# Kernel optimization log

Measured on AMD Instinct MI355X. Metric: run time of the kernel, lower is better.

The kernel has to match this reference:

```python
import jax, jax.numpy as jnp
import numpy as np

EPS = 1e-5

def _add_self_loops(edge_index, n):
    loop = jnp.arange(n, dtype=edge_index.dtype)
    return jnp.concatenate([edge_index, jnp.stack([loop, loop])], axis=1)

def _gcn_norm(row, col, n, dtype):
    # degree of target nodes (with self loops, unit edge weights)
    deg = jax.ops.segment_sum(jnp.ones(row.shape[0], dtype=dtype), col, num_segments=n)
    dinv = jnp.where(deg > 0, deg ** -0.5, 0.0).astype(dtype)
    return dinv[row] * dinv[col]  # [E]

def _propagate(xw, row, col, ew, n):
    # gather -> scale -> scatter-add
    msgs = ew[:, None] * xw[row]          # [E, C]
    return jax.ops.segment_sum(msgs, col, num_segments=n)  # [N, C]

def _batchnorm(x, gamma, beta):
    mu = jnp.mean(x, axis=0)
    var = jnp.var(x, axis=0)
    return (x - mu) * jax.lax.rsqrt(var + EPS) * gamma + beta

def setup_inputs() -> dict:
    key = jax.random.key(0)
    ks = jax.random.split(key, 10)
    N, C_in, C_h, C_out, E = 50000, 128, 128, 1, 600000
    x = jax.random.normal(ks[0], (N, C_in), dtype=jnp.float32)
    edge_index = jax.random.randint(ks[1], (2, E), 0, N, dtype=jnp.int64)
    s = 1.0 / np.sqrt(C_in)
    return {
        "x": x,
        "edge_index": edge_index,
        "gcn_w": jax.random.uniform(ks[2], (C_in, C_h), jnp.float32, -s, s),
        "gcn_b": jnp.zeros((C_h,), jnp.float32),
        "bn1_g": jnp.ones((C_h,), jnp.float32),
        "bn1_b": jnp.zeros((C_h,), jnp.float32),
        "dcn_w": jax.random.uniform(ks[3], (C_h, C_h), jnp.float32, -s, s),
        "dcn_b": jnp.zeros((C_h,), jnp.float32),
        "bn3_g": jnp.ones((C_h,), jnp.float32),
        "bn3_b": jnp.zeros((C_h,), jnp.float32),
        "out_w": jax.random.uniform(ks[4], (2 * C_h, C_out), jnp.float32, -s, s),
        "out_b": jnp.zeros((C_out,), jnp.float32),
    }

def reference(x, edge_index, gcn_w, gcn_b, bn1_g, bn1_b, dcn_w, dcn_b, bn3_g, bn3_b, out_w, out_b):
    n = x.shape[0]
    ei = _add_self_loops(edge_index, n)
    row, col = ei[0], ei[1]
    ew = _gcn_norm(row, col, n, x.dtype)

    # GCNConv: lin -> normalized aggregate -> bias
    h = _propagate(x @ gcn_w, row, col, ew, n) + gcn_b
    h = _batchnorm(h, bn1_g, bn1_b)

    # DegGNNConv: lin -> normalized aggregate -> elementwise gate with input -> bias
    out = _propagate(h @ dcn_w, row, col, ew, n)
    out = out * h + dcn_b
    out = _batchnorm(out, bn3_g, bn3_b)
    # dropout is identity in eval mode

    xc = jnp.concatenate([h, out], axis=-1)  # [N, 2*C_h]
    return xc @ out_w + out_b
```

## Files before the change

kernel.cpp:

```cpp
#include <hip/hip_runtime.h>
#include <hip/hip_bf16.h>
#include <cstdint>


typedef __attribute__((ext_vector_type(8))) short bf16x8;
typedef __attribute__((ext_vector_type(4))) float f32x4;

__device__ __forceinline__ ushort f2bf(float f) {
    union { float f; unsigned u; } c; c.f = f;
    unsigned u = c.u;
    return (ushort)((u + 0x7fffu + ((u >> 16) & 1u)) >> 16);
}
__device__ __forceinline__ unsigned pack2bf(float a, float b) {
    return (unsigned)f2bf(a) | ((unsigned)f2bf(b) << 16);
}
__device__ __forceinline__ float bflo(unsigned u) {
    union { unsigned i; float f; } c; c.i = u << 16; return c.f;
}
__device__ __forceinline__ float bfhi(unsigned u) {
    union { unsigned i; float f; } c; c.i = u & 0xffff0000u; return c.f;
}

__global__ void zero_kernel(uint4* __restrict__ p, int nwords) {
    int i = blockIdx.x * blockDim.x + threadIdx.x;
    if (i < nwords) p[i] = (uint4){0u, 0u, 0u, 0u};
}

__global__ void convert_kernel(const void* __restrict__ ei, int E,
                               int* __restrict__ count) {
    const int* e32 = (const int*)ei;
    bool is64 = ((e32[1] | e32[3] | e32[5] | e32[7]) == 0);
    int stride = gridDim.x * blockDim.x;
    for (int e = blockIdx.x * blockDim.x + threadIdx.x; e < E; e += stride) {
        int c = is64 ? (int)((const long long*)ei)[E + e] : e32[E + e];
        atomicAdd(&count[c], 1);
    }
}

__global__ __launch_bounds__(256) void bsum_kernel(const int* __restrict__ count,
                                                   int* __restrict__ bsum, int n) {
    int t = threadIdx.x;
    int i0 = blockIdx.x * 1024 + t * 4;
    int s = 0;
    if (i0 + 4 <= n) {
        int4 v = *(const int4*)&count[i0];
        s = v.x + v.y + v.z + v.w;
    } else {
        for (int i = i0; i < n; i++) s += count[i];
    }
    __shared__ int ls[256];
    ls[t] = s;
    __syncthreads();
    for (int off = 128; off > 0; off >>= 1) {
        if (t < off) ls[t] += ls[t + off];
        __syncthreads();
    }
    if (t == 0) bsum[blockIdx.x] = ls[0];
}

__global__ void scanb_kernel(int* __restrict__ bsum, int nb) {
    __shared__ int sm[1024];
    int t = threadIdx.x;
    int v = (t < nb) ? bsum[t] : 0;
    sm[t] = v;
    __syncthreads();
    for (int off = 1; off < 1024; off <<= 1) {
        int a = (t >= off) ? sm[t - off] : 0;
        __syncthreads();
        sm[t] += a;
        __syncthreads();
    }
    if (t < nb) bsum[t] = sm[t] - v;
}

__global__ __launch_bounds__(256) void emit_kernel(const int* __restrict__ count,
                                                   const int* __restrict__ bbase,
                                                   int* __restrict__ base, int n) {
    int t = threadIdx.x;
    int i0 = blockIdx.x * 1024 + t * 4;
    int v[4];
    int s = 0;
    if (i0 + 4 <= n) {
        int4 q = *(const int4*)&count[i0];
        v[0] = q.x; v[1] = q.y; v[2] = q.z; v[3] = q.w;
        s = v[0] + v[1] + v[2] + v[3];
    } else {
        #pragma unroll
        for (int k = 0; k < 4; k++) {
            int i = i0 + k;
            v[k] = (i < n) ? count[i] : 0;
            s += v[k];
        }
    }
    __shared__ int sm[256];
    sm[t] = s;
    __syncthreads();
    for (int off = 1; off < 256; off <<= 1) {
        int a = (t >= off) ? sm[t - off] : 0;
        __syncthreads();
        sm[t] += a;
        __syncthreads();
    }
    int run = bbase[blockIdx.x] + sm[t] - s;
    #pragma unroll
    for (int k = 0; k < 4; k++) {
        int i = i0 + k;
        if (i < n) {
            base[i] = run;
            run += v[k];
        }
    }
}

__global__ void scatter_kernel(const void* __restrict__ ei, int E,
                               const int* __restrict__ base, int* __restrict__ cursor,
                               const int* __restrict__ count,
                               unsigned* __restrict__ esrc) {
    const int* e32 = (const int*)ei;
    bool is64 = ((e32[1] | e32[3] | e32[5] | e32[7]) == 0);
    int stride = gridDim.x * blockDim.x;
    for (int e = blockIdx.x * blockDim.x + threadIdx.x; e < E; e += stride) {
        int r, c;
        if (is64) {
            r = (int)((const long long*)ei)[e];
            c = (int)((const long long*)ei)[E + e];
        } else {
            r = e32[e];
            c = e32[E + e];
        }
        int pos = base[c] + atomicAdd(&cursor[c], 1);
        unsigned deg = (unsigned)count[r];
        esrc[pos] = (deg << 24) | ((unsigned)r << 6);
    }
}

__global__ void wtrans_kernel(const float* __restrict__ W1, ushort* __restrict__ WT1,
                              const float* __restrict__ W2, ushort* __restrict__ WT2) {
    int b = blockIdx.x;
    const float* W = (b < 64) ? W1 : W2;
    ushort* WT = (b < 64) ? WT1 : WT2;
    int t = (b & 63) * 256 + threadIdx.x;
    int c = t >> 7, k = t & 127;
    WT[t] = f2bf(W[k * 128 + c]);
}

__global__ __launch_bounds__(256) void gemm_mfma_kernel(const float* __restrict__ Xf,
                                                        const ushort* __restrict__ Xb,
                                                        const ushort* __restrict__ WT,
                                                        const float* __restrict__ ab,
                                                        ushort* __restrict__ Ybf, int n) {
    __shared__ ushort Wl[128 * 136];
    int t = threadIdx.x;
    for (int idx = t * 8; idx < 128 * 128; idx += 256 * 8) {
        int c = idx >> 7;
        int k = idx & 127;
        *(uint4*)&Wl[c * 136 + k] = *(const uint4*)&WT[idx];
    }
    __syncthreads();

    int wid = t >> 6;
    int lane = t & 63;
    int m0 = blockIdx.x * 64 + wid * 16;
    if (m0 >= n) return;
    int row = m0 + (lane & 15);
    int rc = row < n ? row : n - 1;
    int kg = (lane >> 4) * 8;

    f32x4 acc[8];
    #pragma unroll
    for (int i = 0; i < 8; i++) acc[i] = (f32x4){0.f, 0.f, 0.f, 0.f};

    #pragma unroll
    for (int ks = 0; ks < 4; ks++) {
        int k0 = ks * 32 + kg;
        bf16x8 a;
        if (Xb) {
            uint4 q = *(const uint4*)&Xb[(size_t)rc * 128 + k0];
            float f0 = bflo(q.x), f1 = bfhi(q.x), f2 = bflo(q.y), f3 = bfhi(q.y);
            float f4 = bflo(q.z), f5 = bfhi(q.z), f6 = bflo(q.w), f7 = bfhi(q.w);
            float4 alo = *(const float4*)&ab[k0];
            float4 ahi = *(const float4*)&ab[k0 + 4];
            float4 blo = *(const float4*)&ab[128 + k0];
            float4 bhi = *(const float4*)&ab[128 + k0 + 4];
            a[0] = (short)f2bf(alo.x * f0 + blo.x);
            a[1] = (short)f2bf(alo.y * f1 + blo.y);
            a[2] = (short)f2bf(alo.z * f2 + blo.z);
            a[3] = (short)f2bf(alo.w * f3 + blo.w);
            a[4] = (short)f2bf(ahi.x * f4 + bhi.x);
            a[5] = (short)f2bf(ahi.y * f5 + bhi.y);
            a[6] = (short)f2bf(ahi.z * f6 + bhi.z);
            a[7] = (short)f2bf(ahi.w * f7 + bhi.w);
        } else {
            const float* xr = &Xf[(size_t)rc * 128];
            float4 lo = *(const float4*)&xr[k0];
            float4 hi = *(const float4*)&xr[k0 + 4];
            a[0] = (short)f2bf(lo.x); a[1] = (short)f2bf(lo.y);
            a[2] = (short)f2bf(lo.z); a[3] = (short)f2bf(lo.w);
            a[4] = (short)f2bf(hi.x); a[5] = (short)f2bf(hi.y);
            a[6] = (short)f2bf(hi.z); a[7] = (short)f2bf(hi.w);
        }
        #pragma unroll
        for (int nt = 0; nt < 8; nt++) {
            int c = nt * 16 + (lane & 15);
            bf16x8 b = *(bf16x8*)&Wl[c * 136 + k0];
            acc[nt] = __builtin_amdgcn_mfma_f32_16x16x32_bf16(a, b, acc[nt], 0, 0, 0);
        }
    }

    int ro = m0 + (lane >> 4) * 4;
    int co = lane & 15;
    #pragma unroll
    for (int nt = 0; nt < 8; nt++) {
        #pragma unroll
        for (int i = 0; i < 4; i++) {
            int r = ro + i;
            if (r < n) Ybf[(size_t)r * 128 + nt * 16 + co] = f2bf(acc[nt][i]);
        }
    }
}

__global__ __launch_bounds__(256) void prop_kernel(const uint4* __restrict__ XW4,
                            const int* __restrict__ base,
                            const int* __restrict__ count, const unsigned* __restrict__ esrc,
                            const uint4* __restrict__ B1q, const float* __restrict__ ab1,
                            uint4* __restrict__ outq,
                            float* __restrict__ psum, float* __restrict__ psq,
                            int n, int gate) {
    int wave4 = (int)((blockIdx.x * blockDim.x + threadIdx.x) >> 6);
    int lane = threadIdx.x & 63;
    int wid = threadIdx.x >> 6;
    int g = lane >> 4;
    int p = lane & 15;
    int node = wave4 * 4 + g;
    bool valid = node < n;
    int nc = valid ? node : n - 1;
    int b = 0, cnt = 0;
    if (valid) { b = base[node]; cnt = count[node]; }
    float din = rsqrtf((float)(cnt + 1));

    uint4 vs = XW4[(size_t)nc * 16 + p];

    float ax[8];
    #pragma unroll
    for (int k = 0; k < 8; k++) ax[k] = 0.f;

    for (int i = 0; i < cnt; i += 4) {
        unsigned pj[4];
        uint4 vj[4];
        #pragma unroll
        for (int j = 0; j < 4; j++) {
            int e = i + j;
            pj[j] = esrc[b + (e < cnt ? e : cnt - 1)];
        }
        #pragma unroll
        for (int j = 0; j < 4; j++)
            vj[j] = XW4[((pj[j] & 0xFFFFFFu) >> 2) + p];
        #pragma unroll
        for (int j = 0; j < 4; j++) {
            float w = (i + j < cnt) ? rsqrtf((float)((pj[j] >> 24) + 1)) : 0.f;
            ax[0] += w * bflo(vj[j].x); ax[1] += w * bfhi(vj[j].x);
            ax[2] += w * bflo(vj[j].y); ax[3] += w * bfhi(vj[j].y);
            ax[4] += w * bflo(vj[j].z); ax[5] += w * bfhi(vj[j].z);
            ax[6] += w * bflo(vj[j].w); ax[7] += w * bfhi(vj[j].w);
        }
    }

    float sv[8];
    sv[0] = bflo(vs.x); sv[1] = bfhi(vs.x); sv[2] = bflo(vs.y); sv[3] = bfhi(vs.y);
    sv[4] = bflo(vs.z); sv[5] = bfhi(vs.z); sv[6] = bflo(vs.w); sv[7] = bfhi(vs.w);
    #pragma unroll
    for (int k = 0; k < 8; k++) ax[k] = din * (ax[k] + din * sv[k]);

    float vv[8];
    if (gate) {
        uint4 b1 = B1q[(size_t)nc * 16 + p];
        float bv[8];
        bv[0] = bflo(b1.x); bv[1] = bfhi(b1.x); bv[2] = bflo(b1.y); bv[3] = bfhi(b1.y);
        bv[4] = bflo(b1.z); bv[5] = bfhi(b1.z); bv[6] = bflo(b1.w); bv[7] = bfhi(b1.w);
        int c0 = p * 8;
        #pragma unroll
        for (int k = 0; k < 8; k++) {
            float h = ab1[c0 + k] * bv[k] + ab1[128 + c0 + k];
            vv[k] = ax[k] * h;
        }
    } else {
        #pragma unroll
        for (int k = 0; k < 8; k++) vv[k] = ax[k];
    }

    if (valid) {
        uint4 o;
        o.x = pack2bf(vv[0], vv[1]);
        o.y = pack2bf(vv[2], vv[3]);
        o.z = pack2bf(vv[4], vv[5]);
        o.w = pack2bf(vv[6], vv[7]);
        outq[(size_t)node * 16 + p] = o;
    } else {
        #pragma unroll
        for (int k = 0; k < 8; k++) vv[k] = 0.f;
    }

    float ss[8], qq[8];
    #pragma unroll
    for (int k = 0; k < 8; k++) { ss[k] = vv[k]; qq[k] = vv[k] * vv[k]; }
    #pragma unroll
    for (int k = 0; k < 8; k++) {
        ss[k] += __shfl_xor(ss[k], 16); qq[k] += __shfl_xor(qq[k], 16);
        ss[k] += __shfl_xor(ss[k], 32); qq[k] += __shfl_xor(qq[k], 32);
    }
    __shared__ float sm_s[4][128], sm_q[4][128];
    if (g == 0) {
        int c0 = p * 8;
        #pragma unroll
        for (int k = 0; k < 8; k++) {
            sm_s[wid][c0 + k] = ss[k];
            sm_q[wid][c0 + k] = qq[k];
        }
    }
    __syncthreads();
    if (threadIdx.x < 128) {
        int c = threadIdx.x;
        float s = sm_s[0][c] + sm_s[1][c] + sm_s[2][c] + sm_s[3][c];
        float q2 = sm_q[0][c] + sm_q[1][c] + sm_q[2][c] + sm_q[3][c];
        int slot = (blockIdx.x & 63) * 128;
        atomicAdd(&psum[slot + c], s);
        atomicAdd(&psq[slot + c], q2);
    }
}

__global__ void reduce_ab_kernel(const float* __restrict__ psum, const float* __restrict__ psq,
                                 const float* __restrict__ g, const float* __restrict__ beta,
                                 float* __restrict__ ab, int n) {
    int c = threadIdx.x;
    float s = 0.f, s2 = 0.f;
    for (int r = 0; r < 64; r++) {
        s += psum[r * 128 + c];
        s2 += psq[r * 128 + c];
    }
    float invn = 1.f / (float)n;
    float mu = s * invn;
    float var = s2 * invn - mu * mu;
    float a = g[c] * rsqrtf(var + 1e-5f);
    ab[c] = a;
    ab[128 + c] = beta[c] - mu * a;
}

__global__ void final_kernel(const unsigned* __restrict__ B1bf, const unsigned* __restrict__ B2bf,
                             const float* __restrict__ ab1, const float* __restrict__ ab3,
                             const float* __restrict__ ow, const float* __restrict__ ob,
                             float* __restrict__ out, int n) {
    int wave = (int)((blockIdx.x * blockDim.x + threadIdx.x) >> 6);
    int lane = threadIdx.x & 63;
    if (wave >= n) return;
    int c0 = 2 * lane, c1 = c0 + 1;
    unsigned b1 = B1bf[(size_t)wave * 64 + lane];
    unsigned b2 = B2bf[(size_t)wave * 64 + lane];
    float h0 = ab1[c0] * bflo(b1) + ab1[128 + c0];
    float h1 = ab1[c1] * bfhi(b1) + ab1[128 + c1];
    float o0 = ab3[c0] * bflo(b2) + ab3[128 + c0];
    float o1 = ab3[c1] * bfhi(b2) + ab3[128 + c1];
    float partial = h0 * ow[c0] + h1 * ow[c1] + o0 * ow[128 + c0] + o1 * ow[128 + c1];
    #pragma unroll
    for (int off = 32; off > 0; off >>= 1) partial += __shfl_down(partial, off);
    if (lane == 0) out[wave] = partial + ob[0];
}

extern "C" void kernel_launch(void* const* d_in, const int* in_sizes, int n_in,
                              void* d_out, int out_size, void* d_ws, size_t ws_size,
                              hipStream_t stream) {
    const float* x     = (const float*)d_in[0];
    const void*  ei    = d_in[1];
    const float* gcn_w = (const float*)d_in[2];
    const float* bn1_g = (const float*)d_in[4];
    const float* bn1_b = (const float*)d_in[5];
    const float* dcn_w = (const float*)d_in[6];
    const float* bn3_g = (const float*)d_in[8];
    const float* bn3_b = (const float*)d_in[9];
    const float* out_w = (const float*)d_in[10];
    const float* out_b = (const float*)d_in[11];
    float* out = (float*)d_out;

    int N = in_sizes[0] / 128;
    int E = in_sizes[1] / 2;
    size_t N128 = (size_t)N * 128;

    ushort* Abf   = (ushort*)d_ws;
    ushort* B1bf  = Abf + N128;
    ushort* B2bf  = B1bf + N128;
    unsigned* esrc = (unsigned*)(B2bf + N128);
    int*   base  = (int*)(esrc + E);
    int*   bsum  = base + N;
    ushort* WT1  = (ushort*)(bsum + 1024);
    ushort* WT2  = WT1 + 16384;
    float* ab1   = (float*)(WT2 + 16384);
    float* ab3   = ab1 + 256;
    int*   count  = (int*)(ab3 + 256);
    int*   cursor = count + N;
    float* psum1  = (float*)(cursor + N);
    float* psq1   = psum1 + 8192;
    float* psum3  = psq1 + 8192;
    float* psq3   = psum3 + 8192;

    size_t zero_bytes = (size_t)((char*)(psq3 + 8192) - (char*)count);
    int zwords = (int)(zero_bytes / 16);
    zero_kernel<<<(zwords + 255) / 256, 256, 0, stream>>>((uint4*)count, zwords);

    int egrid = (E + 255) / 256;
    if (egrid > 2048) egrid = 2048;
    int nb = (N + 1023) / 1024;
    int ggrid = (N + 63) / 64;
    int pgrid = (N + 15) / 16;
    int fgrid = (N + 3) / 4;

    convert_kernel<<<egrid, 256, 0, stream>>>(ei, E, count);
    bsum_kernel<<<nb, 256, 0, stream>>>(count, bsum, N);
    scanb_kernel<<<1, 1024, 0, stream>>>(bsum, nb);
    emit_kernel<<<nb, 256, 0, stream>>>(count, bsum, base, N);
    scatter_kernel<<<egrid, 256, 0, stream>>>(ei, E, base, cursor, count, esrc);
    wtrans_kernel<<<128, 256, 0, stream>>>(gcn_w, WT1, dcn_w, WT2);

    gemm_mfma_kernel<<<ggrid, 256, 0, stream>>>(x, nullptr, WT1, nullptr, Abf, N);
    prop_kernel<<<pgrid, 256, 0, stream>>>((const uint4*)Abf, base, count, esrc,
                                           nullptr, nullptr, (uint4*)B1bf,
                                           psum1, psq1, N, 0);
    reduce_ab_kernel<<<1, 128, 0, stream>>>(psum1, psq1, bn1_g, bn1_b, ab1, N);

    gemm_mfma_kernel<<<ggrid, 256, 0, stream>>>(nullptr, B1bf, WT2, ab1, Abf, N);
    prop_kernel<<<pgrid, 256, 0, stream>>>((const uint4*)Abf, base, count, esrc,
                                           (const uint4*)B1bf, ab1, (uint4*)B2bf,
                                           psum3, psq3, N, 1);
    reduce_ab_kernel<<<1, 128, 0, stream>>>(psum3, psq3, bn3_g, bn3_b, ab3, N);

    final_kernel<<<fgrid, 256, 0, stream>>>((const unsigned*)B1bf, (const unsigned*)B2bf,
                                            ab1, ab3, out_w, out_b, out, N);
}
```

Measured before the change: 172.2 us.

## Merge independent setup kernels into heterogeneous launches and drop cursor array

The weight transpose now runs as extra blocks inside the degree-count kernel. The edge scatter and the first GEMM share one launch, with block index choosing the role. The separate cursor array is gone: scatter atomically bumps base[c] directly, and prop recovers the start offset as base minus count. This cuts launches and serialization gaps and lets the GEMM overlap the atomic-bound scatter. In exchange, the fused kernel carries GEMM shared-memory usage into the scatter blocks, which may reduce their occupancy.

```diff
diff --git a/kernel.cpp b/kernel.cpp
--- a/kernel.cpp
+++ b/kernel.cpp
@@ -26,12 +26,23 @@
     if (i < nwords) p[i] = (uint4){0u, 0u, 0u, 0u};
 }
 
-__global__ void convert_kernel(const void* __restrict__ ei, int E,
-                               int* __restrict__ count) {
+__global__ void fuse1_kernel(const void* __restrict__ ei, int E,
+                             int* __restrict__ count, int cgrid,
+                             const float* __restrict__ W1, ushort* __restrict__ WT1,
+                             const float* __restrict__ W2, ushort* __restrict__ WT2) {
+    if (blockIdx.x >= cgrid) {
+        int b = blockIdx.x - cgrid;
+        const float* W = (b < 64) ? W1 : W2;
+        ushort* WT = (b < 64) ? WT1 : WT2;
+        int t = (b & 63) * 256 + threadIdx.x;
+        int c = t >> 7, k = t & 127;
+        WT[t] = f2bf(W[k * 128 + c]);
+        return;
+    }
     const int* e32 = (const int*)ei;
     bool is64 = ((e32[1] | e32[3] | e32[5] | e32[7]) == 0);
-    int stride = gridDim.x * blockDim.x;
-    for (int e = blockIdx.x * blockDim.x + threadIdx.x; e < E; e += stride) {
+    int stride = cgrid * 256;
+    for (int e = blockIdx.x * 256 + threadIdx.x; e < E; e += stride) {
         int c = is64 ? (int)((const long long*)ei)[E + e] : e32[E + e];
         atomicAdd(&count[c], 1);
     }
@@ -112,40 +123,84 @@
     }
 }
 
-__global__ void scatter_kernel(const void* __restrict__ ei, int E,
-                               const int* __restrict__ base, int* __restrict__ cursor,
-                               const int* __restrict__ count,
-                               unsigned* __restrict__ esrc) {
-    const int* e32 = (const int*)ei;
-    bool is64 = ((e32[1] | e32[3] | e32[5] | e32[7]) == 0);
-    int stride = gridDim.x * blockDim.x;
-    for (int e = blockIdx.x * blockDim.x + threadIdx.x; e < E; e += stride) {
-        int r, c;
-        if (is64) {
-            r = (int)((const long long*)ei)[e];
-            c = (int)((const long long*)ei)[E + e];
-        } else {
-            r = e32[e];
-            c = e32[E + e];
-        }
-        int pos = base[c] + atomicAdd(&cursor[c], 1);
-        unsigned deg = (unsigned)count[r];
-        esrc[pos] = (deg << 24) | ((unsigned)r << 6);
-    }
-}
-
-__global__ void wtrans_kernel(const float* __restrict__ W1, ushort* __restrict__ WT1,
-                              const float* __restrict__ W2, ushort* __restrict__ WT2) {
-    int b = blockIdx.x;
-    const float* W = (b < 64) ? W1 : W2;
-    ushort* WT = (b < 64) ? WT1 : WT2;
-    int t = (b & 63) * 256 + threadIdx.x;
-    int c = t >> 7, k = t & 127;
-    WT[t] = f2bf(W[k * 128 + c]);
-}
-
-__global__ __launch_bounds__(256) void gemm_mfma_kernel(const float* __restrict__ Xf,
-                                                        const ushort* __restrict__ Xb,
+__global__ __launch_bounds__(256) void fuse2_kernel(const void* __restrict__ ei, int E,
+                             int* __restrict__ base, const int* __restrict__ count,
+                             unsigned* __restrict__ esrc, int sgrid,
+                             const float* __restrict__ Xf, const ushort* __restrict__ WT,
+                             ushort* __restrict__ Ybf, int n) {
+    __shared__ ushort Wl[128 * 136];
+    if (blockIdx.x < sgrid) {
+        const int* e32 = (const int*)ei;
+        bool is64 = ((e32[1] | e32[3] | e32[5] | e32[7]) == 0);
+        int stride = sgrid * 256;
+        for (int e = blockIdx.x * 256 + threadIdx.x; e < E; e += stride) {
+            int r, c;
+            if (is64) {
+                r = (int)((const long long*)ei)[e];
+                c = (int)((const long long*)ei)[E + e];
+            } else {
+                r = e32[e];
+                c = e32[E + e];
+            }
+            int pos = atomicAdd(&base[c], 1);
+            unsigned deg = (unsigned)count[r];
+            esrc[pos] = (deg << 24) | ((unsigned)r << 6);
+        }
+        return;
+    }
+    int gb = blockIdx.x - sgrid;
+    int t = threadIdx.x;
+    for (int idx = t * 8; idx < 128 * 128; idx += 256 * 8) {
+        int c = idx >> 7;
+        int k = idx & 127;
+        *(uint4*)&Wl[c * 136 + k] = *(const uint4*)&WT[idx];
+    }
+    __syncthreads();
+
+    int wid = t >> 6;
+    int lane = t & 63;
+    int m0 = gb * 64 + wid * 16;
+    if (m0 >= n) return;
+    int row = m0 + (lane & 15);
+    int rc = row < n ? row : n - 1;
+    int kg = (lane >> 4) * 8;
+
+    f32x4 acc[8];
+    #pragma unroll
+    for (int i = 0; i < 8; i++) acc[i] = (f32x4){0.f, 0.f, 0.f, 0.f};
+
+    #pragma unroll
+    for (int ks = 0; ks < 4; ks++) {
+        int k0 = ks * 32 + kg;
+        const float* xr = &Xf[(size_t)rc * 128];
+        float4 lo = *(const float4*)&xr[k0];
+        float4 hi = *(const float4*)&xr[k0 + 4];
+        bf16x8 a;
+        a[0] = (short)f2bf(lo.x); a[1] = (short)f2bf(lo.y);
+        a[2] = (short)f2bf(lo.z); a[3] = (short)f2bf(lo.w);
+        a[4] = (short)f2bf(hi.x); a[5] = (short)f2bf(hi.y);
+        a[6] = (short)f2bf(hi.z); a[7] = (short)f2bf(hi.w);
+        #pragma unroll
+        for (int nt = 0; nt < 8; nt++) {
+            int c = nt * 16 + (lane & 15);
+            bf16x8 b = *(bf16x8*)&Wl[c * 136 + k0];
+            acc[nt] = __builtin_amdgcn_mfma_f32_16x16x32_bf16(a, b, acc[nt], 0, 0, 0);
+        }
+    }
+
+    int ro = m0 + (lane >> 4) * 4;
+    int co = lane & 15;
+    #pragma unroll
+    for (int nt = 0; nt < 8; nt++) {
+        #pragma unroll
+        for (int i = 0; i < 4; i++) {
+            int r = ro + i;
+            if (r < n) Ybf[(size_t)r * 128 + nt * 16 + co] = f2bf(acc[nt][i]);
+        }
+    }
+}
+
+__global__ __launch_bounds__(256) void gemm_mfma_kernel(const ushort* __restrict__ Xb,
                                                         const ushort* __restrict__ WT,
                                                         const float* __restrict__ ab,
                                                         ushort* __restrict__ Ybf, int n) {
@@ -173,32 +228,22 @@
     #pragma unroll
     for (int ks = 0; ks < 4; ks++) {
         int k0 = ks * 32 + kg;
+        uint4 q = *(const uint4*)&Xb[(size_t)rc * 128 + k0];
+        float f0 = bflo(q.x), f1 = bfhi(q.x), f2 = bflo(q.y), f3 = bfhi(q.y);
+        float f4 = bflo(q.z), f5 = bfhi(q.z), f6 = bflo(q.w), f7 = bfhi(q.w);
+        float4 alo = *(const float4*)&ab[k0];
+        float4 ahi = *(const float4*)&ab[k0 + 4];
+        float4 blo = *(const float4*)&ab[128 + k0];
+        float4 bhi = *(const float4*)&ab[128 + k0 + 4];
         bf16x8 a;
-        if (Xb) {
-            uint4 q = *(const uint4*)&Xb[(size_t)rc * 128 + k0];
-            float f0 = bflo(q.x), f1 = bfhi(q.x), f2 = bflo(q.y), f3 = bfhi(q.y);
-            float f4 = bflo(q.z), f5 = bfhi(q.z), f6 = bflo(q.w), f7 = bfhi(q.w);
-            float4 alo = *(const float4*)&ab[k0];
-            float4 ahi = *(const float4*)&ab[k0 + 4];
-            float4 blo = *(const float4*)&ab[128 + k0];
-            float4 bhi = *(const float4*)&ab[128 + k0 + 4];
-            a[0] = (short)f2bf(alo.x * f0 + blo.x);
-            a[1] = (short)f2bf(alo.y * f1 + blo.y);
-            a[2] = (short)f2bf(alo.z * f2 + blo.z);
-            a[3] = (short)f2bf(alo.w * f3 + blo.w);
-            a[4] = (short)f2bf(ahi.x * f4 + bhi.x);
-            a[5] = (short)f2bf(ahi.y * f5 + bhi.y);
-            a[6] = (short)f2bf(ahi.z * f6 + bhi.z);
-            a[7] = (short)f2bf(ahi.w * f7 + bhi.w);
-        } else {
-            const float* xr = &Xf[(size_t)rc * 128];
-            float4 lo = *(const float4*)&xr[k0];
-            float4 hi = *(const float4*)&xr[k0 + 4];
-            a[0] = (short)f2bf(lo.x); a[1] = (short)f2bf(lo.y);
-            a[2] = (short)f2bf(lo.z); a[3] = (short)f2bf(lo.w);
-            a[4] = (short)f2bf(hi.x); a[5] = (short)f2bf(hi.y);
-            a[6] = (short)f2bf(hi.z); a[7] = (short)f2bf(hi.w);
-        }
+        a[0] = (short)f2bf(alo.x * f0 + blo.x);
+        a[1] = (short)f2bf(alo.y * f1 + blo.y);
+        a[2] = (short)f2bf(alo.z * f2 + blo.z);
+        a[3] = (short)f2bf(alo.w * f3 + blo.w);
+        a[4] = (short)f2bf(ahi.x * f4 + bhi.x);
+        a[5] = (short)f2bf(ahi.y * f5 + bhi.y);
+        a[6] = (short)f2bf(ahi.z * f6 + bhi.z);
+        a[7] = (short)f2bf(ahi.w * f7 + bhi.w);
         #pragma unroll
         for (int nt = 0; nt < 8; nt++) {
             int c = nt * 16 + (lane & 15);
@@ -235,7 +280,7 @@
     bool valid = node < n;
     int nc = valid ? node : n - 1;
     int b = 0, cnt = 0;
-    if (valid) { b = base[node]; cnt = count[node]; }
+    if (valid) { cnt = count[node]; b = base[node] - cnt; }
     float din = rsqrtf((float)(cnt + 1));
 
     uint4 vs = XW4[(size_t)nc * 16 + p];
@@ -395,8 +440,7 @@
     float* ab1   = (float*)(WT2 + 16384);
     float* ab3   = ab1 + 256;
     int*   count  = (int*)(ab3 + 256);
-    int*   cursor = count + N;
-    float* psum1  = (float*)(cursor + N);
+    float* psum1  = (float*)(count + N);
     float* psq1   = psum1 + 8192;
     float* psum3  = psq1 + 8192;
     float* psq3   = psum3 + 8192;
@@ -405,27 +449,27 @@
     int zwords = (int)(zero_bytes / 16);
     zero_kernel<<<(zwords + 255) / 256, 256, 0, stream>>>((uint4*)count, zwords);
 
-    int egrid = (E + 255) / 256;
-    if (egrid > 2048) egrid = 2048;
+    int cgrid = (E + 255) / 256;
+    if (cgrid > 2048) cgrid = 2048;
     int nb = (N + 1023) / 1024;
     int ggrid = (N + 63) / 64;
     int pgrid = (N + 15) / 16;
     int fgrid = (N + 3) / 4;
 
-    convert_kernel<<<egrid, 256, 0, stream>>>(ei, E, count);
+    fuse1_kernel<<<cgrid + 128, 256, 0, stream>>>(ei, E, count, cgrid,
+                                                  gcn_w, WT1, dcn_w, WT2);
     bsum_kernel<<<nb, 256, 0, stream>>>(count, bsum, N);
     scanb_kernel<<<1, 1024, 0, stream>>>(bsum, nb);
     emit_kernel<<<nb, 256, 0, stream>>>(count, bsum, base, N);
-    scatter_kernel<<<egrid, 256, 0, stream>>>(ei, E, base, cursor, count, esrc);
-    wtrans_kernel<<<128, 256, 0, stream>>>(gcn_w, WT1, dcn_w, WT2);
-
-    gemm_mfma_kernel<<<ggrid, 256, 0, stream>>>(x, nullptr, WT1, nullptr, Abf, N);
+    fuse2_kernel<<<cgrid + ggrid, 256, 0, stream>>>(ei, E, base, count, esrc, cgrid,
+                                                    x, WT1, Abf, N);
+
     prop_kernel<<<pgrid, 256, 0, stream>>>((const uint4*)Abf, base, count, esrc,
                                            nullptr, nullptr, (uint4*)B1bf,
                                            psum1, psq1, N, 0);
     reduce_ab_kernel<<<1, 128, 0, stream>>>(psum1, psq1, bn1_g, bn1_b, ab1, N);
 
-    gemm_mfma_kernel<<<ggrid, 256, 0, stream>>>(nullptr, B1bf, WT2, ab1, Abf, N);
+    gemm_mfma_kernel<<<ggrid, 256, 0, stream>>>(B1bf, WT2, ab1, Abf, N);
     prop_kernel<<<pgrid, 256, 0, stream>>>((const uint4*)Abf, base, count, esrc,
                                            (const uint4*)B1bf, ab1, (uint4*)B2bf,
                                            psum3, psq3, N, 1);
```

New measurement: 169.6 us (median of 3 runs). Within noise of the previous version (-1.6%).
